# Kernel tuning notes

Hardware: AMD Instinct MI355X
Metric: run time of the kernel (lower is better)

## Reference

```python
import jax, jax.numpy as jnp
import numpy as np

NUM_NODES, WINDOW, DIM, B = 50000, 8, 256, 8192


def setup_inputs() -> dict:
    key = jax.random.key(0)
    k1, k2, k3, k4, k5, k6 = jax.random.split(key, 6)
    return {
        "bank": jax.random.normal(k1, (NUM_NODES, WINDOW, DIM), dtype=jnp.float32),
        "timestamps": jax.random.uniform(k2, (NUM_NODES, WINDOW), dtype=jnp.float32),
        "neighbor_repr": jax.random.normal(k3, (B, DIM), dtype=jnp.float32),
        "t": jax.random.uniform(k4, (B,), dtype=jnp.float32) * 1000.0,
        "ptr": jax.random.randint(k5, (NUM_NODES,), 0, 1000000, dtype=jnp.int64) if jax.config.jax_enable_x64 else jax.random.randint(k5, (NUM_NODES,), 0, 1000000, dtype=jnp.int32),
        "idx": jax.random.randint(k6, (B,), 0, NUM_NODES, dtype=jnp.int32),
    }


def reference(bank, timestamps, neighbor_repr, t, ptr, idx):
    """Vectorized equivalent of NeighborhoodEvolutionBank.write().

    The torch loop writes batch elements sequentially: the k-th occurrence of a
    node index within the batch lands in slot (ptr[node] + k) % window, and ptr
    is bumped once per occurrence. We reproduce that by computing, for each
    batch element, its rank among earlier duplicates of the same index.
    """
    window = bank.shape[1]
    # rank[bi] = number of j < bi with idx[j] == idx[bi]  (B x B, B=8192 -> 64M bool, fine)
    eq = idx[:, None] == idx[None, :]
    rank = jnp.sum(jnp.tril(eq, k=-1), axis=1).astype(ptr.dtype)  # [B]
    slot = (ptr[idx] + rank) % window                              # [B]

    bank_new = bank.at[idx, slot].set(neighbor_repr)               # fused scatter write
    ts_new = timestamps.at[idx, slot].set(t.astype(timestamps.dtype))
    ptr_new = ptr.at[idx].add(1)
    return bank_new, ts_new, ptr_new
```

## Files before the change

kernel.cpp:

```cpp
#include <hip/hip_runtime.h>

#define NUM_NODES 50000
#define WINDOW 8
#define DIM 256
#define BATCH 8192

__global__ void count_kernel(const int* __restrict__ idx, int* __restrict__ count) {
    int bi = blockIdx.x * blockDim.x + threadIdx.x;
    if (bi < BATCH) atomicAdd(&count[idx[bi]], 1);
}

__global__ void rank_kernel(const int* __restrict__ idx, const int* __restrict__ ptr,
                            const int* __restrict__ count, int* __restrict__ winner) {
    __shared__ int sidx[BATCH];
    __shared__ int anyneed;
    int tid = threadIdx.x;
    int bi  = blockIdx.x * blockDim.x + tid;

    int node = idx[bi];
    int c    = count[node];
    bool need = (c > 1);

    if (tid == 0) anyneed = 0;
    __syncthreads();
    if (need) anyneed = 1;
    __syncthreads();

    if (anyneed) {
        for (int j = tid; j < BATCH; j += blockDim.x) sidx[j] = idx[j];
        __syncthreads();
    }

    int rank = 0;
    if (need) {
        for (int j = 0; j < bi; ++j) rank += (sidx[j] == node);
    }

    if (rank >= c - WINDOW) {
        int slot = (ptr[node] + rank) & (WINDOW - 1);
        winner[node * WINDOW + slot] = bi;
    }
}

__global__ void __launch_bounds__(256)
fused_copy_kernel(const float4* __restrict__ bank4,
                  const float*  __restrict__ timestamps,
                  const float4* __restrict__ nrep4,
                  const float*  __restrict__ t,
                  const int*    __restrict__ winner,
                  float4* __restrict__ out_bank4,
                  float*  __restrict__ out_ts) {
    const long total = (long)NUM_NODES * WINDOW * (DIM / 4);
    const long nth   = (long)gridDim.x * blockDim.x;
    for (long i = (long)blockIdx.x * blockDim.x + threadIdx.x; i < total; i += nth) {
        int  row = (int)(i >> 6);
        int  w   = winner[row];
        float4 v = (w >= 0) ? nrep4[(long)w * (DIM / 4) + (i & 63)] : bank4[i];
        out_bank4[i] = v;
        if ((i & 63) == 0)
            out_ts[row] = (w >= 0) ? t[w] : timestamps[row];
    }
}

__global__ void ptr_kernel(const int* __restrict__ ptr, const int* __restrict__ count,
                           float* __restrict__ out_ptr) {
    int n = blockIdx.x * blockDim.x + threadIdx.x;
    if (n < NUM_NODES) out_ptr[n] = (float)(ptr[n] + count[n]);
}

extern "C" void kernel_launch(void* const* d_in, const int* in_sizes, int n_in,
                              void* d_out, int out_size, void* d_ws, size_t ws_size,
                              hipStream_t stream) {
    const float* bank       = (const float*)d_in[0];
    const float* timestamps = (const float*)d_in[1];
    const float* nrep       = (const float*)d_in[2];
    const float* t          = (const float*)d_in[3];
    const int*   ptr        = (const int*)  d_in[4];
    const int*   idx        = (const int*)  d_in[5];

    float* out_bank = (float*)d_out;
    float* out_ts   = out_bank + (size_t)NUM_NODES * WINDOW * DIM;
    float* out_ptr  = out_ts   + (size_t)NUM_NODES * WINDOW;

    int* count  = (int*)d_ws;
    int* winner = count + NUM_NODES;

    hipMemsetAsync(count, 0, NUM_NODES * sizeof(int), stream);
    hipMemsetAsync(winner, 0xFF, (size_t)NUM_NODES * WINDOW * sizeof(int), stream);

    count_kernel<<<(BATCH + 255) / 256, 256, 0, stream>>>(idx, count);
    rank_kernel<<<BATCH / 256, 256, 0, stream>>>(idx, ptr, count, winner);

    fused_copy_kernel<<<2048, 256, 0, stream>>>(
        (const float4*)bank, timestamps, (const float4*)nrep, t, winner,
        (float4*)out_bank, out_ts);

    ptr_kernel<<<(NUM_NODES + 255) / 256, 256, 0, stream>>>(ptr, count, out_ptr);
}
```

Before: 241.9 us.

## Merge memsets, count and rank into one single-block prep kernel

Replaces two memsets and the count and rank kernels with a single 1024-thread block. It clears the workspace, counts occurrences, and computes ranks only among duplicate indices, compacted into shared memory. The winner table shrinks from int to short, and the ptr output is folded into the copy kernel. This removes several launches and cuts winner-table traffic, but the prep stage now runs on a single workgroup, clearing 400K shorts serially.

```diff
diff --git a/kernel.cpp b/kernel.cpp
--- a/kernel.cpp
+++ b/kernel.cpp
@@ -4,68 +4,67 @@
 #define WINDOW 8
 #define DIM 256
 #define BATCH 8192
+#define NROWS (NUM_NODES * WINDOW)
+#define BANK4 ((long)NROWS * (DIM / 4))
 
-__global__ void count_kernel(const int* __restrict__ idx, int* __restrict__ count) {
-    int bi = blockIdx.x * blockDim.x + threadIdx.x;
-    if (bi < BATCH) atomicAdd(&count[idx[bi]], 1);
-}
+__global__ void __launch_bounds__(1024)
+prep_kernel(const int* __restrict__ idx, const int* __restrict__ ptr,
+            int* __restrict__ count, short* __restrict__ winner) {
+    __shared__ int spos [BATCH];
+    __shared__ int snode[BATCH];
+    __shared__ int scnt [BATCH];
+    __shared__ int sndup;
+    const int tid = threadIdx.x;
 
-__global__ void rank_kernel(const int* __restrict__ idx, const int* __restrict__ ptr,
-                            const int* __restrict__ count, int* __restrict__ winner) {
-    __shared__ int sidx[BATCH];
-    __shared__ int anyneed;
-    int tid = threadIdx.x;
-    int bi  = blockIdx.x * blockDim.x + tid;
-
-    int node = idx[bi];
-    int c    = count[node];
-    bool need = (c > 1);
-
-    if (tid == 0) anyneed = 0;
-    __syncthreads();
-    if (need) anyneed = 1;
+    int* winner_i = (int*)winner;
+    for (int i = tid; i < NUM_NODES; i += 1024) count[i] = 0;
+    for (int i = tid; i < NROWS / 2; i += 1024) winner_i[i] = 0xFFFFFFFF;
+    if (tid == 0) sndup = 0;
     __syncthreads();
 
-    if (anyneed) {
-        for (int j = tid; j < BATCH; j += blockDim.x) sidx[j] = idx[j];
-        __syncthreads();
+    for (int bi = tid; bi < BATCH; bi += 1024) atomicAdd(&count[idx[bi]], 1);
+    __syncthreads();
+
+    for (int bi = tid; bi < BATCH; bi += 1024) {
+        int node = idx[bi];
+        int c    = atomicAdd(&count[node], 0);
+        if (c == 1) {
+            winner[node * WINDOW + (ptr[node] & (WINDOW - 1))] = (short)bi;
+        } else {
+            int k = atomicAdd(&sndup, 1);
+            spos[k] = bi; snode[k] = node; scnt[k] = c;
+        }
     }
+    __syncthreads();
 
-    int rank = 0;
-    if (need) {
-        for (int j = 0; j < bi; ++j) rank += (sidx[j] == node);
-    }
-
-    if (rank >= c - WINDOW) {
-        int slot = (ptr[node] + rank) & (WINDOW - 1);
-        winner[node * WINDOW + slot] = bi;
+    const int n = sndup;
+    for (int k = tid; k < n; k += 1024) {
+        int p = spos[k], node = snode[k], rank = 0;
+        for (int m = 0; m < n; ++m)
+            rank += (spos[m] < p && snode[m] == node);
+        if (rank >= scnt[k] - WINDOW)
+            winner[node * WINDOW + ((ptr[node] + rank) & (WINDOW - 1))] = (short)p;
     }
 }
 
 __global__ void __launch_bounds__(256)
-fused_copy_kernel(const float4* __restrict__ bank4,
-                  const float*  __restrict__ timestamps,
-                  const float4* __restrict__ nrep4,
-                  const float*  __restrict__ t,
-                  const int*    __restrict__ winner,
-                  float4* __restrict__ out_bank4,
-                  float*  __restrict__ out_ts) {
-    const long total = (long)NUM_NODES * WINDOW * (DIM / 4);
-    const long nth   = (long)gridDim.x * blockDim.x;
-    for (long i = (long)blockIdx.x * blockDim.x + threadIdx.x; i < total; i += nth) {
-        int  row = (int)(i >> 6);
-        int  w   = winner[row];
+fused_copy_kernel(const float4* __restrict__ bank4, const float* __restrict__ ts,
+                  const float4* __restrict__ nrep4, const float* __restrict__ t,
+                  const short* __restrict__ winner,
+                  const int* __restrict__ ptr, const int* __restrict__ count,
+                  float4* __restrict__ out_bank4, float* __restrict__ out_ts,
+                  float* __restrict__ out_ptr) {
+    const long tid = (long)blockIdx.x * blockDim.x + threadIdx.x;
+    const long nth = (long)gridDim.x * blockDim.x;
+    for (long i = tid; i < BANK4; i += nth) {
+        int row = (int)(i >> 6);
+        int w   = winner[row];
         float4 v = (w >= 0) ? nrep4[(long)w * (DIM / 4) + (i & 63)] : bank4[i];
         out_bank4[i] = v;
         if ((i & 63) == 0)
-            out_ts[row] = (w >= 0) ? t[w] : timestamps[row];
+            out_ts[row] = (w >= 0) ? t[w] : ts[row];
     }
-}
-
-__global__ void ptr_kernel(const int* __restrict__ ptr, const int* __restrict__ count,
-                           float* __restrict__ out_ptr) {
-    int n = blockIdx.x * blockDim.x + threadIdx.x;
-    if (n < NUM_NODES) out_ptr[n] = (float)(ptr[n] + count[n]);
+    if (tid < NUM_NODES) out_ptr[tid] = (float)(ptr[tid] + count[tid]);
 }
 
 extern "C" void kernel_launch(void* const* d_in, const int* in_sizes, int n_in,
@@ -82,18 +81,12 @@
     float* out_ts   = out_bank + (size_t)NUM_NODES * WINDOW * DIM;
     float* out_ptr  = out_ts   + (size_t)NUM_NODES * WINDOW;
 
-    int* count  = (int*)d_ws;
-    int* winner = count + NUM_NODES;
+    int*   count  = (int*)d_ws;
+    short* winner = (short*)(count + NUM_NODES);
 
-    hipMemsetAsync(count, 0, NUM_NODES * sizeof(int), stream);
-    hipMemsetAsync(winner, 0xFF, (size_t)NUM_NODES * WINDOW * sizeof(int), stream);
-
-    count_kernel<<<(BATCH + 255) / 256, 256, 0, stream>>>(idx, count);
-    rank_kernel<<<BATCH / 256, 256, 0, stream>>>(idx, ptr, count, winner);
+    prep_kernel<<<1, 1024, 0, stream>>>(idx, ptr, count, winner);
 
     fused_copy_kernel<<<2048, 256, 0, stream>>>(
         (const float4*)bank, timestamps, (const float4*)nrep, t, winner,
-        (float4*)out_bank, out_ts);
-
-    ptr_kernel<<<(NUM_NODES + 255) / 256, 256, 0, stream>>>(ptr, count, out_ptr);
+        ptr, count, (float4*)out_bank, out_ts, out_ptr);
 }
```

After: 382.6 us. 1.58x slower.
